# Kernel tuning notes

Measured on AMD Instinct MI355X. Metric: run time of the kernel, lower is better.

## Reference

```python
import jax, jax.numpy as jnp
import numpy as np

D = 768
H = 16
DK = D // H
DFF = 3072
POOL = 100
NCLS = 7
EPS = 1e-6


def layer_norm(x, a, b):
    # torch: (x - mean) / (std + eps), std unbiased (ddof=1)
    mean = jnp.mean(x, axis=-1, keepdims=True)
    var = jnp.sum((x - mean) ** 2, axis=-1, keepdims=True) / (x.shape[-1] - 1)
    return a * (x - mean) / (jnp.sqrt(var) + EPS) + b


def mha(x, Wq, bq, Wk, bk, Wv, bv, Wo, bo):
    B, S, _ = x.shape
    def split(h):
        return h.reshape(B, S, H, DK).transpose(0, 2, 1, 3)  # [B,H,S,DK]
    q = split(x @ Wq + bq)
    k = split(x @ Wk + bk)
    v = split(x @ Wv + bv)
    scores = jnp.einsum('bhqd,bhkd->bhqk', q, k) / jnp.sqrt(jnp.float32(DK))
    p = jax.nn.softmax(scores, axis=-1)
    o = jnp.einsum('bhqk,bhkd->bhqd', p, v)
    o = o.transpose(0, 2, 1, 3).reshape(B, S, D)
    return o @ Wo + bo


def setup_inputs() -> dict:
    key = jax.random.key(0)
    ks = jax.random.split(key, 24)
    B, S = 8, 1023
    s = 0.02
    inp = {
        'text_features': jax.random.normal(ks[0], (B, S, D), jnp.float32),
        'prompt_pool': jax.random.normal(ks[1], (POOL, D), jnp.float32),
        'cls_token': jax.random.normal(ks[2], (1, 1, D), jnp.float32),
        'Wq': jax.random.normal(ks[3], (D, D), jnp.float32) * s,
        'bq': jnp.zeros((D,), jnp.float32),
        'Wk': jax.random.normal(ks[4], (D, D), jnp.float32) * s,
        'bk': jnp.zeros((D,), jnp.float32),
        'Wv': jax.random.normal(ks[5], (D, D), jnp.float32) * s,
        'bv': jnp.zeros((D,), jnp.float32),
        'Wo': jax.random.normal(ks[6], (D, D), jnp.float32) * s,
        'bo': jnp.zeros((D,), jnp.float32),
        'ln1_a': jnp.ones((D,), jnp.float32),
        'ln1_b': jnp.zeros((D,), jnp.float32),
        'ln2_a': jnp.ones((D,), jnp.float32),
        'ln2_b': jnp.zeros((D,), jnp.float32),
        'W1': jax.random.normal(ks[7], (D, DFF), jnp.float32) * s,
        'b1': jnp.zeros((DFF,), jnp.float32),
        'W2': jax.random.normal(ks[8], (DFF, D), jnp.float32) * s,
        'b2': jnp.zeros((D,), jnp.float32),
        'lnf_a': jnp.ones((D,), jnp.float32),
        'lnf_b': jnp.zeros((D,), jnp.float32),
        'Wpool': jax.random.normal(ks[9], (D, POOL), jnp.float32) * s,
        'bpool': jnp.zeros((POOL,), jnp.float32),
        'Wcls': jax.random.normal(ks[10], (D, NCLS), jnp.float32) * s,
        'bcls': jnp.zeros((NCLS,), jnp.float32),
    }
    return inp


def reference(text_features, prompt_pool, cls_token, Wq, bq, Wk, bk, Wv, bv, Wo, bo,
              ln1_a, ln1_b, ln2_a, ln2_b, W1, b1, W2, b2, lnf_a, lnf_b,
              Wpool, bpool, Wcls, bcls):
    B = text_features.shape[0]
    x = jnp.concatenate([jnp.broadcast_to(cls_token, (B, 1, D)), text_features], axis=1)
    # EncoderLayer (N=1), dropout in eval mode (identity)
    x = x + mha(layer_norm(x, ln1_a, ln1_b), Wq, bq, Wk, bk, Wv, bv, Wo, bo)
    h = layer_norm(x, ln2_a, ln2_b)
    x = x + (jax.nn.relu(h @ W1 + b1) @ W2 + b2)
    x = layer_norm(x, lnf_a, lnf_b)
    cls = x[:, 0, :]  # [B, D]
    probabilities = jax.nn.softmax(cls @ Wpool + bpool, axis=1)  # [B, POOL]
    class_logits = cls @ Wcls + bcls  # [B, NCLS]
    class_probs = jax.nn.softmax(class_logits, axis=1)
    entropy = -jnp.sum(class_probs * jnp.log(class_probs + 1e-9), axis=1)
    max_entropy = jnp.log(jnp.float32(7.0))
    norm_ent = entropy / max_entropy
    adjusted_k = jnp.clip(jnp.floor(1.0 + norm_ent * (POOL - 1)).astype(jnp.int32), 1, POOL)  # [B]
    # full descending top-k (jit-friendly: pad to POOL instead of data-dependent max_k)
    _, top_idx = jax.lax.top_k(probabilities, POOL)  # [B, POOL]
    gathered = prompt_pool[top_idx]  # [B, POOL, D]
    keep = (jnp.arange(POOL)[None, :] < adjusted_k[:, None]).astype(prompt_pool.dtype)
    selected_prompts = gathered * keep[:, :, None]
    return (selected_prompts, class_logits)
```

## Files before the change

### kernel.cpp

```cpp
#include <hip/hip_runtime.h>


#define OUT_CLS_OFF 614400

__device__ __forceinline__ float bsum256(float v, float* red) {
    int lane = threadIdx.x & 63, w = threadIdx.x >> 6;
#pragma unroll
    for (int off = 1; off < 64; off <<= 1) v += __shfl_xor(v, off);
    __syncthreads();
    if (lane == 0) red[w] = v;
    __syncthreads();
    return red[0] + red[1] + red[2] + red[3];
}

__global__ __launch_bounds__(256) void prep_a(
    const float* __restrict__ clsT, const float* __restrict__ ga,
    const float* __restrict__ gb, const float* __restrict__ Wq,
    const float* __restrict__ bq, const float* __restrict__ Wk,
    float* __restrict__ q0, float* __restrict__ colw, int* __restrict__ cnts)
{
    __shared__ float ys[768];
    __shared__ float red[4];
    __shared__ float4 partA[16][17];
    __shared__ float4 partB[16][17];
    int t = threadIdx.x;
    if (blockIdx.x == 0 && t < 16) cnts[t] = 0;
    if (blockIdx.x < 12) {
        float a0 = clsT[t], a1 = clsT[t + 256], a2 = clsT[t + 512];
        float mean = bsum256(a0 + a1 + a2, red) * (1.0f / 768.0f);
        float d0 = a0 - mean, d1 = a1 - mean, d2 = a2 - mean;
        float var = bsum256(d0 * d0 + d1 * d1 + d2 * d2, red) * (1.0f / 767.0f);
        float den = sqrtf(var) + 1e-6f;
        ys[t]       = (ga[t] * d0) / den + gb[t];
        ys[t + 256] = (ga[t + 256] * d1) / den + gb[t + 256];
        ys[t + 512] = (ga[t + 512] * d2) / den + gb[t + 512];
        __syncthreads();
        int c = blockIdx.x * 64 + (t & 15) * 4;
        int kq = t >> 4;
        float4 acc = {0.f, 0.f, 0.f, 0.f};
#pragma unroll 8
        for (int i = 0; i < 48; ++i) {
            int k = kq * 48 + i;
            float4 w = *(const float4*)&Wq[(size_t)k * 768 + c];
            float y = ys[k];
            acc.x = fmaf(y, w.x, acc.x); acc.y = fmaf(y, w.y, acc.y);
            acc.z = fmaf(y, w.z, acc.z); acc.w = fmaf(y, w.w, acc.w);
        }
        partA[kq][t & 15] = acc;
        __syncthreads();
        if (t < 16) {
            float4 s = {0.f, 0.f, 0.f, 0.f};
#pragma unroll
            for (int i = 0; i < 16; ++i) {
                float4 v = partA[i][t];
                s.x += v.x; s.y += v.y; s.z += v.z; s.w += v.w;
            }
            int cc = blockIdx.x * 64 + t * 4;
            float4 b4 = *(const float4*)&bq[cc];
            q0[cc] = s.x + b4.x; q0[cc + 1] = s.y + b4.y;
            q0[cc + 2] = s.z + b4.z; q0[cc + 3] = s.w + b4.w;
        }
    } else {
        int c = (blockIdx.x - 12) * 64 + (t & 15) * 4;
        int kq = t >> 4;
        float4 aa = {0.f, 0.f, 0.f, 0.f}, ab = {0.f, 0.f, 0.f, 0.f};
#pragma unroll 8
        for (int i = 0; i < 48; ++i) {
            int k = kq * 48 + i;
            float4 w = *(const float4*)&Wk[(size_t)k * 768 + c];
            float g = ga[k], h = gb[k];
            aa.x = fmaf(g, w.x, aa.x); aa.y = fmaf(g, w.y, aa.y);
            aa.z = fmaf(g, w.z, aa.z); aa.w = fmaf(g, w.w, aa.w);
            ab.x = fmaf(h, w.x, ab.x); ab.y = fmaf(h, w.y, ab.y);
            ab.z = fmaf(h, w.z, ab.z); ab.w = fmaf(h, w.w, ab.w);
        }
        partA[kq][t & 15] = aa;
        partB[kq][t & 15] = ab;
        __syncthreads();
        if (t < 16) {
            float4 sa = {0.f, 0.f, 0.f, 0.f}, sb = {0.f, 0.f, 0.f, 0.f};
#pragma unroll
            for (int i = 0; i < 16; ++i) {
                float4 va = partA[i][t], vb = partB[i][t];
                sa.x += va.x; sa.y += va.y; sa.z += va.z; sa.w += va.w;
                sb.x += vb.x; sb.y += vb.y; sb.z += vb.z; sb.w += vb.w;
            }
            int cc = (blockIdx.x - 12) * 64 + t * 4;
            *(float4*)&colw[cc] = sa;
            *(float4*)&colw[768 + cc] = sb;
        }
    }
}

__global__ __launch_bounds__(256) void prep_b(
    const float* __restrict__ Wk, const float* __restrict__ bk,
    const float* __restrict__ q0, const float* __restrict__ colw,
    float* __restrict__ wkqc)
{
    __shared__ float qs[768];
    int t = threadIdx.x;
    qs[t] = q0[t]; qs[t + 256] = q0[t + 256]; qs[t + 512] = q0[t + 512];
    __syncthreads();
    const float invs = 0.14433756729740643f;
    int kl = t >> 4, h = t & 15;
    int k = blockIdx.x * 16 + kl;
    const float* wr = Wk + (size_t)k * 768 + h * 48;
    const float* qh = qs + h * 48;
    float a = 0.f;
#pragma unroll
    for (int d = 0; d < 48; d += 4) {
        float4 w = *(const float4*)&wr[d];
        a += w.x * qh[d] + w.y * qh[d + 1] + w.z * qh[d + 2] + w.w * qh[d + 3];
    }
    wkqc[k * 16 + h] = a * invs;
    if (blockIdx.x == 0 && t < 16) {
        float cd = 0.f, sa = 0.f, sb = 0.f;
        for (int d = 0; d < 48; ++d) {
            int dd = t * 48 + d;
            cd = fmaf(bk[dd], qs[dd], cd);
            sa = fmaf(colw[dd], qs[dd], sa);
            sb = fmaf(colw[768 + dd], qs[dd], sb);
        }
        wkqc[12304 + t] = sa * invs;
        wkqc[12320 + t] = sb * invs + cd * invs;
    }
}

__global__ __launch_bounds__(256) void score_upart(
    const float* __restrict__ tf, const float* __restrict__ clsT,
    const float* __restrict__ ga, const float* __restrict__ wkqc,
    float* __restrict__ up, float* __restrict__ upz, float* __restrict__ upc1)
{
    __shared__ float tr[256][17];
    __shared__ float partw[4][16];
    __shared__ float red[2][4][2];
    __shared__ float wrow[16];
    int t = threadIdx.x;
    int l = t & 63, w = t >> 6;

    float wk0[16], wk1[16], wk2[16];
    {
        const float4* p0 = (const float4*)(wkqc + t * 16);
        const float4* p1 = (const float4*)(wkqc + (t + 256) * 16);
        const float4* p2 = (const float4*)(wkqc + (t + 512) * 16);
#pragma unroll
        for (int q = 0; q < 4; ++q) {
            float4 v0 = p0[q], v1 = p1[q], v2 = p2[q];
            wk0[q * 4] = v0.x; wk0[q * 4 + 1] = v0.y; wk0[q * 4 + 2] = v0.z; wk0[q * 4 + 3] = v0.w;
            wk1[q * 4] = v1.x; wk1[q * 4 + 1] = v1.y; wk1[q * 4 + 2] = v1.z; wk1[q * 4 + 3] = v1.w;
            wk2[q * 4] = v2.x; wk2[q * 4 + 1] = v2.y; wk2[q * 4 + 2] = v2.z; wk2[q * 4 + 3] = v2.w;
        }
    }
    float ga0 = ga[t], ga1 = ga[t + 256], ga2 = ga[t + 512];
    float Sg = wkqc[12304 + (t & 15)];
    float Cg = wkqc[12320 + (t & 15)];

    float acc0[16], acc1[16], acc2[16];
#pragma unroll
    for (int h = 0; h < 16; ++h) { acc0[h] = 0.f; acc1[h] = 0.f; acc2[h] = 0.f; }
    float zacc = 0.f, c1acc = 0.f;

    int b = blockIdx.x & 7, jc = blockIdx.x >> 3;
    int j0 = jc * 32;
    const float* src0 = j0 ? (tf + ((size_t)b * 1023 + (j0 - 1)) * 768) : clsT;
    float x0 = src0[t], x1 = src0[t + 256], x2 = src0[t + 512];

    for (int r = 0; r < 32; ++r) {
        int j = j0 + r;
        float cx0 = x0, cx1 = x1, cx2 = x2;
        if (r < 31) {
            const float* sp = tf + ((size_t)b * 1023 + j) * 768;
            x0 = sp[t]; x1 = sp[t + 256]; x2 = sp[t + 512];
        }
        float s1 = cx0 + cx1 + cx2;
        float s2 = fmaf(cx0, cx0, fmaf(cx1, cx1, cx2 * cx2));
        float g0 = ga0 * cx0, g1 = ga1 * cx1, g2 = ga2 * cx2;
        {
            float dt[16];
#pragma unroll
            for (int h = 0; h < 16; ++h)
                dt[h] = fmaf(g0, wk0[h], fmaf(g1, wk1[h], g2 * wk2[h]));
#pragma unroll
            for (int off = 1; off < 64; off <<= 1) {
                s1 += __shfl_xor(s1, off);
                s2 += __shfl_xor(s2, off);
            }
            if (l == 0) { red[r & 1][w][0] = s1; red[r & 1][w][1] = s2; }
#pragma unroll
            for (int h = 0; h < 16; ++h) tr[t][h] = dt[h];
        }
        __syncthreads();
        {
            int hh = t & 15, ch = t >> 4;
            float v = 0.f;
#pragma unroll
            for (int i = 0; i < 16; ++i) v += tr[ch * 16 + i][hh];
            v += __shfl_xor(v, 16);
            v += __shfl_xor(v, 32);
            if (l < 16) partw[w][l] = v;
        }
        __syncthreads();
        if (t < 16) {
            float dtot = partw[0][t] + partw[1][t] + partw[2][t] + partw[3][t];
            float s1t = red[r & 1][0][0] + red[r & 1][1][0] + red[r & 1][2][0] + red[r & 1][3][0];
            float s2t = red[r & 1][0][1] + red[r & 1][1][1] + red[r & 1][2][1] + red[r & 1][3][1];
            float mean = s1t * (1.0f / 768.0f);
            float var = (s2t - mean * s1t) * (1.0f / 767.0f);
            float rden = 1.0f / (sqrtf(var) + 1e-6f);
            float sv = rden * (dtot - mean * Sg) + Cg;
            float e = expf(sv);
            float wv = e * rden;
            wrow[t] = wv;
            zacc += e;
            c1acc = fmaf(wv, mean, c1acc);
        }
        __syncthreads();
#pragma unroll
        for (int h = 0; h < 16; ++h) {
            float wh = wrow[h];
            acc0[h] = fmaf(wh, cx0, acc0[h]);
            acc1[h] = fmaf(wh, cx1, acc1[h]);
            acc2[h] = fmaf(wh, cx2, acc2[h]);
        }
    }

    float* o = up + (((size_t)b * 32 + jc) * 16) * 768;
#pragma unroll
    for (int h = 0; h < 16; ++h) {
        o[h * 768 + t] = acc0[h];
        o[h * 768 + t + 256] = acc1[h];
        o[h * 768 + t + 512] = acc2[h];
    }
    if (t < 16) {
        upz[((size_t)b * 32 + jc) * 16 + t] = zacc;
        upc1[((size_t)b * 32 + jc) * 16 + t] = c1acc;
    }
}

__global__ __launch_bounds__(256) void o0_k(
    const float* __restrict__ up, const float* __restrict__ upz,
    const float* __restrict__ upc1, const float* __restrict__ ga,
    const float* __restrict__ gb, const float* __restrict__ Wv,
    const float* __restrict__ bv, float* __restrict__ o0)
{
    __shared__ float us[768];
    __shared__ float part[4][64];
    int h = blockIdx.x, b = blockIdx.y, t = threadIdx.x;
    float s0 = 0.f, s1 = 0.f, s2 = 0.f;
#pragma unroll 8
    for (int jc = 0; jc < 32; ++jc) {
        const float* q = up + (((size_t)b * 32 + jc) * 16 + h) * 768;
        s0 += q[t]; s1 += q[t + 256]; s2 += q[t + 512];
    }
    float Z = 0.f, c1r = 0.f;
#pragma unroll 8
    for (int jc = 0; jc < 32; ++jc) {
        Z   += upz[((size_t)b * 32 + jc) * 16 + h];
        c1r += upc1[((size_t)b * 32 + jc) * 16 + h];
    }
    float rz = 1.0f / Z;
    us[t]       = ga[t] * ((s0 - c1r) * rz) + gb[t];
    us[t + 256] = ga[t + 256] * ((s1 - c1r) * rz) + gb[t + 256];
    us[t + 512] = ga[t + 512] * ((s2 - c1r) * rz) + gb[t + 512];
    __syncthreads();
    int dd = t & 63, kg = t >> 6;
    float a = 0.f;
    if (dd < 48) {
#pragma unroll 8
        for (int i = 0; i < 192; ++i) {
            int k = kg * 192 + i;
            a = fmaf(us[k], Wv[(size_t)k * 768 + h * 48 + dd], a);
        }
    }
    part[kg][dd] = a;
    __syncthreads();
    if (t < 48)
        o0[(size_t)b * 768 + h * 48 + t] =
            part[0][t] + part[1][t] + part[2][t] + part[3][t] + bv[h * 48 + t];
}

__global__ __launch_bounds__(256) void x2_k(
    const float* __restrict__ o0, const float* __restrict__ Wo,
    const float* __restrict__ bo, const float* __restrict__ clsT,
    float* __restrict__ x2w)
{
    __shared__ float ys[768];
    __shared__ float4 part[16][17];
    int b = blockIdx.y, t = threadIdx.x;
    const float* xr = o0 + (size_t)b * 768;
    ys[t] = xr[t]; ys[t + 256] = xr[t + 256]; ys[t + 512] = xr[t + 512];
    __syncthreads();
    int c = blockIdx.x * 64 + (t & 15) * 4;
    int kq = t >> 4;
    float4 acc = {0.f, 0.f, 0.f, 0.f};
#pragma unroll 8
    for (int i = 0; i < 48; ++i) {
        int k = kq * 48 + i;
        float4 w = *(const float4*)&Wo[(size_t)k * 768 + c];
        float y = ys[k];
        acc.x = fmaf(y, w.x, acc.x); acc.y = fmaf(y, w.y, acc.y);
        acc.z = fmaf(y, w.z, acc.z); acc.w = fmaf(y, w.w, acc.w);
    }
    part[kq][t & 15] = acc;
    __syncthreads();
    if (t < 16) {
        float4 s = {0.f, 0.f, 0.f, 0.f};
#pragma unroll
        for (int i = 0; i < 16; ++i) {
            float4 v = part[i][t];
            s.x += v.x; s.y += v.y; s.z += v.z; s.w += v.w;
        }
        int cc = blockIdx.x * 64 + t * 4;
        float4 b4 = *(const float4*)&bo[cc];
        float4 r4 = *(const float4*)&clsT[cc];
        float* o = x2w + (size_t)b * 768 + cc;
        o[0] = s.x + b4.x + r4.x; o[1] = s.y + b4.y + r4.y;
        o[2] = s.z + b4.z + r4.z; o[3] = s.w + b4.w + r4.w;
    }
}

__global__ __launch_bounds__(256) void f1_k(
    const float* __restrict__ x2w, const float* __restrict__ ga,
    const float* __restrict__ gb, const float* __restrict__ W1,
    const float* __restrict__ b1, float* __restrict__ f1w)
{
    __shared__ float ys[768];
    __shared__ float red[4];
    __shared__ float4 part[8][33];
    int b = blockIdx.y, t = threadIdx.x;
    const float* xr = x2w + (size_t)b * 768;
    float a0 = xr[t], a1 = xr[t + 256], a2 = xr[t + 512];
    float mean = bsum256(a0 + a1 + a2, red) * (1.0f / 768.0f);
    float d0 = a0 - mean, d1 = a1 - mean, d2 = a2 - mean;
    float var = bsum256(d0 * d0 + d1 * d1 + d2 * d2, red) * (1.0f / 767.0f);
    float den = sqrtf(var) + 1e-6f;
    ys[t]       = (ga[t] * d0) / den + gb[t];
    ys[t + 256] = (ga[t + 256] * d1) / den + gb[t + 256];
    ys[t + 512] = (ga[t + 512] * d2) / den + gb[t + 512];
    __syncthreads();
    int c = blockIdx.x * 128 + (t & 31) * 4;
    int kq = t >> 5;
    float4 acc = {0.f, 0.f, 0.f, 0.f};
#pragma unroll 8
    for (int i = 0; i < 96; ++i) {
        int k = kq * 96 + i;
        float4 w = *(const float4*)&W1[(size_t)k * 3072 + c];
        float y = ys[k];
        acc.x = fmaf(y, w.x, acc.x); acc.y = fmaf(y, w.y, acc.y);
        acc.z = fmaf(y, w.z, acc.z); acc.w = fmaf(y, w.w, acc.w);
    }
    part[kq][t & 31] = acc;
    __syncthreads();
    if (t < 32) {
        float4 s = {0.f, 0.f, 0.f, 0.f};
#pragma unroll
        for (int i = 0; i < 8; ++i) {
            float4 v = part[i][t];
            s.x += v.x; s.y += v.y; s.z += v.z; s.w += v.w;
        }
        int cc = blockIdx.x * 128 + t * 4;
        float4 b4 = *(const float4*)&b1[cc];
        float* o = f1w + (size_t)b * 3072 + cc;
        o[0] = fmaxf(s.x + b4.x, 0.f); o[1] = fmaxf(s.y + b4.y, 0.f);
        o[2] = fmaxf(s.z + b4.z, 0.f); o[3] = fmaxf(s.w + b4.w, 0.f);
    }
}

__global__ __launch_bounds__(256) void x3_k(
    const float* __restrict__ f1w, const float* __restrict__ W2,
    const float* __restrict__ b2, const float* __restrict__ x2w,
    float* __restrict__ x3w)
{
    __shared__ float ys[3072];
    __shared__ float4 part[16][17];
    int b = blockIdx.y, t = threadIdx.x;
    const float* xr = f1w + (size_t)b * 3072;
    for (int i = t; i < 3072; i += 256) ys[i] = xr[i];
    __syncthreads();
    int c = blockIdx.x * 64 + (t & 15) * 4;
    int kq = t >> 4;
    float4 acc = {0.f, 0.f, 0.f, 0.f};
#pragma unroll 8
    for (int i = 0; i < 192; ++i) {
        int k = kq * 192 + i;
        float4 w = *(const float4*)&W2[(size_t)k * 768 + c];
        float y = ys[k];
        acc.x = fmaf(y, w.x, acc.x); acc.y = fmaf(y, w.y, acc.y);
        acc.z = fmaf(y, w.z, acc.z); acc.w = fmaf(y, w.w, acc.w);
    }
    part[kq][t & 15] = acc;
    __syncthreads();
    if (t < 16) {
        float4 s = {0.f, 0.f, 0.f, 0.f};
#pragma unroll
        for (int i = 0; i < 16; ++i) {
            float4 v = part[i][t];
            s.x += v.x; s.y += v.y; s.z += v.z; s.w += v.w;
        }
        int cc = blockIdx.x * 64 + t * 4;
        float4 b4 = *(const float4*)&b2[cc];
        const float* x2r = x2w + (size_t)b * 768 + cc;
        float* o = x3w + (size_t)b * 768 + cc;
        o[0] = x2r[0] + s.x + b4.x; o[1] = x2r[1] + s.y + b4.y;
        o[2] = x2r[2] + s.z + b4.z; o[3] = x2r[3] + s.w + b4.w;
    }
}

__global__ __launch_bounds__(256) void logits_part(
    const float* __restrict__ x3w, const float* __restrict__ ga,
    const float* __restrict__ gb, const float* __restrict__ Wpool,
    const float* __restrict__ Wcls, double* __restrict__ lp,
    const float* __restrict__ bpool, const float* __restrict__ bcls,
    float* __restrict__ out, int* __restrict__ topw, int* __restrict__ kkw,
    int* __restrict__ cnts)
{
    __shared__ float ys[768];
    __shared__ float red[4];
    __shared__ double sPd[100];
    __shared__ double sC7d[7];
    __shared__ int sOld;
    int kg = blockIdx.x, b = blockIdx.y, t = threadIdx.x;
    const float* xr = x3w + (size_t)b * 768;
    float a0 = xr[t], a1 = xr[t + 256], a2 = xr[t + 512];
    float mean = bsum256(a0 + a1 + a2, red) * (1.0f / 768.0f);
    float d0 = a0 - mean, d1 = a1 - mean, d2 = a2 - mean;
    float var = bsum256(d0 * d0 + d1 * d1 + d2 * d2, red) * (1.0f / 767.0f);
    float den = sqrtf(var) + 1e-6f;
    ys[t]       = (ga[t] * d0) / den + gb[t];
    ys[t + 256] = (ga[t + 256] * d1) / den + gb[t + 256];
    ys[t + 512] = (ga[t + 512] * d2) / den + gb[t + 512];
    __syncthreads();
    int kbase = kg * 96;
    if (t < 100) {
        double a = 0.0;
#pragma unroll 8
        for (int i = 0; i < 96; ++i) {
            int k = kbase + i;
            a = fma((double)ys[k], (double)Wpool[k * 100 + t], a);
        }
        lp[((size_t)b * 8 + kg) * 112 + t] = a;
    } else if (t < 107) {
        int c = t - 100;
        double a = 0.0;
#pragma unroll 8
        for (int i = 0; i < 96; ++i) {
            int k = kbase + i;
            a = fma((double)ys[k], (double)Wcls[k * 7 + c], a);
        }
        lp[((size_t)b * 8 + kg) * 112 + t] = a;
    }

    __syncthreads();
    __threadfence();
    if (t == 0)
        sOld = __hip_atomic_fetch_add(&cnts[b], 1, __ATOMIC_ACQ_REL,
                                      __HIP_MEMORY_SCOPE_AGENT);
    __syncthreads();
    if (sOld != 7) return;

    if (t < 107) {
        double a = (t < 100) ? (double)bpool[t] : (double)bcls[t - 100];
#pragma unroll
        for (int g = 0; g < 8; ++g) a += lp[((size_t)b * 8 + g) * 112 + t];
        if (t < 100) sPd[t] = a;
        else {
            sC7d[t - 100] = a;
            out[OUT_CLS_OFF + b * 7 + (t - 100)] = (float)a;
        }
    }
    __syncthreads();
    if (t == 0) {
        double m7 = sC7d[0];
        for (int j = 1; j < 7; ++j) m7 = fmax(m7, sC7d[j]);
        double es[7]; double z = 0.0;
        for (int j = 0; j < 7; ++j) { es[j] = exp(sC7d[j] - m7); z += es[j]; }
        double ent = 0.0;
        for (int j = 0; j < 7; ++j) { double pr = es[j] / z; ent -= pr * log(pr + 1e-9); }
        double ne = ent / log(7.0);
        int kk = (int)floor(1.0 + ne * 99.0);
        kkw[b] = kk < 1 ? 1 : (kk > 100 ? 100 : kk);
    }
    if (t < 100) {
        double pi = sPd[t];
        int r = 0;
#pragma unroll 4
        for (int j = 0; j < 100; ++j) {
            double pj = sPd[j];
            r += (pj > pi) || (pj == pi && j < t);
        }
        topw[b * 100 + r] = t;
    }
}

__global__ __launch_bounds__(192) void gather_k(
    const float* __restrict__ pool, const int* __restrict__ topw,
    const int* __restrict__ kkw, float* __restrict__ out)
{
    int r = blockIdx.x, b = blockIdx.y, t = threadIdx.x;
    int idx = topw[b * 100 + r];
    bool keep = r < kkw[b];
    const float4* src = (const float4*)(pool + (size_t)idx * 768);
    float4* dst = (float4*)(out + (size_t)b * 76800 + (size_t)r * 768);
    float4 z = {0.f, 0.f, 0.f, 0.f};
    dst[t] = keep ? src[t] : z;
}

extern "C" void kernel_launch(void* const* d_in, const int* in_sizes, int n_in,
                              void* d_out, int out_size, void* d_ws, size_t ws_size,
                              hipStream_t stream) {
    (void)in_sizes; (void)n_in; (void)out_size; (void)ws_size;
    const float* tf    = (const float*)d_in[0];
    const float* pool  = (const float*)d_in[1];
    const float* clsT  = (const float*)d_in[2];
    const float* Wq    = (const float*)d_in[3];
    const float* bq    = (const float*)d_in[4];
    const float* Wk    = (const float*)d_in[5];
    const float* bk    = (const float*)d_in[6];
    const float* Wv    = (const float*)d_in[7];
    const float* bv    = (const float*)d_in[8];
    const float* Wo    = (const float*)d_in[9];
    const float* bo    = (const float*)d_in[10];
    const float* ln1a  = (const float*)d_in[11];
    const float* ln1b  = (const float*)d_in[12];
    const float* ln2a  = (const float*)d_in[13];
    const float* ln2b  = (const float*)d_in[14];
    const float* W1    = (const float*)d_in[15];
    const float* b1    = (const float*)d_in[16];
    const float* W2    = (const float*)d_in[17];
    const float* b2    = (const float*)d_in[18];
    const float* lnfa  = (const float*)d_in[19];
    const float* lnfb  = (const float*)d_in[20];
    const float* Wpool = (const float*)d_in[21];
    const float* bpool = (const float*)d_in[22];
    const float* Wcls  = (const float*)d_in[23];
    const float* bcls  = (const float*)d_in[24];
    float* out = (float*)d_out;
    char* ws = (char*)d_ws;

    float*  wkqc  = (float*)(ws + 0);
    float*  q0    = (float*)(ws + 49408);
    float*  colw  = (float*)(ws + 52480);
    float*  up    = (float*)(ws + 58624);
    float*  upz   = (float*)(ws + 12641536);
    float*  upc1  = (float*)(ws + 12657920);
    float*  o0    = (float*)(ws + 12674304);
    float*  x2w   = (float*)(ws + 12698880);
    float*  f1w   = (float*)(ws + 12723456);
    float*  x3w   = (float*)(ws + 12821760);
    int*    topw  = (int*)(ws + 12846336);
    int*    kkw   = (int*)(ws + 12849536);
    double* lp    = (double*)(ws + 12849568);
    int*    cnts  = (int*)(ws + 12906912);

    prep_a<<<24, 256, 0, stream>>>(clsT, ln1a, ln1b, Wq, bq, Wk, q0, colw, cnts);
    prep_b<<<48, 256, 0, stream>>>(Wk, bk, q0, colw, wkqc);
    score_upart<<<256, 256, 0, stream>>>(tf, clsT, ln1a, wkqc, up, upz, upc1);
    o0_k<<<dim3(16, 8), 256, 0, stream>>>(up, upz, upc1, ln1a, ln1b, Wv, bv, o0);
    x2_k<<<dim3(12, 8), 256, 0, stream>>>(o0, Wo, bo, clsT, x2w);
    f1_k<<<dim3(24, 8), 256, 0, stream>>>(x2w, ln2a, ln2b, W1, b1, f1w);
    x3_k<<<dim3(12, 8), 256, 0, stream>>>(f1w, W2, b2, x2w, x3w);
    logits_part<<<dim3(8, 8), 256, 0, stream>>>(x3w, lnfa, lnfb, Wpool, Wcls,
                                                lp, bpool, bcls, out, topw,
                                                kkw, cnts);
    gather_k<<<dim3(100, 8), 192, 0, stream>>>(pool, topw, kkw, out);
}
```

Before: 115.6 us.

## Halve score_upart chunk size, double grid, and defer accumulation to drop a barrier

Splits the 1024-row sequence into 64 chunks of 16 rows per batch, so score_upart launches 512 blocks instead of 256 and more of the GPU's compute units have work. The weighted-accumulate step for each row moves to the next iteration using a double-buffered wrow, which removes one __syncthreads per row. It also adds a launch-bounds occupancy hint. The cost is twice as many partial buffers (workspace offsets shift) and a 64-way reduction in o0_k instead of 32-way.

```diff
diff --git a/kernel.cpp b/kernel.cpp
--- a/kernel.cpp
+++ b/kernel.cpp
@@ -126,7 +126,7 @@
     }
 }
 
-__global__ __launch_bounds__(256) void score_upart(
+__global__ __launch_bounds__(256, 2) void score_upart(
     const float* __restrict__ tf, const float* __restrict__ clsT,
     const float* __restrict__ ga, const float* __restrict__ wkqc,
     float* __restrict__ up, float* __restrict__ upz, float* __restrict__ upc1)
@@ -134,7 +134,7 @@
     __shared__ float tr[256][17];
     __shared__ float partw[4][16];
     __shared__ float red[2][4][2];
-    __shared__ float wrow[16];
+    __shared__ float wrow[2][16];
     int t = threadIdx.x;
     int l = t & 63, w = t >> 6;
 
@@ -161,20 +161,21 @@
     float zacc = 0.f, c1acc = 0.f;
 
     int b = blockIdx.x & 7, jc = blockIdx.x >> 3;
-    int j0 = jc * 32;
+    int j0 = jc * 16;
     const float* src0 = j0 ? (tf + ((size_t)b * 1023 + (j0 - 1)) * 768) : clsT;
-    float x0 = src0[t], x1 = src0[t + 256], x2 = src0[t + 512];
-
-    for (int r = 0; r < 32; ++r) {
+    float xc0 = src0[t], xc1 = src0[t + 256], xc2 = src0[t + 512];
+    float xp0 = 0.f, xp1 = 0.f, xp2 = 0.f;
+
+    for (int r = 0; r < 16; ++r) {
         int j = j0 + r;
-        float cx0 = x0, cx1 = x1, cx2 = x2;
-        if (r < 31) {
+        float s1 = xc0 + xc1 + xc2;
+        float s2 = fmaf(xc0, xc0, fmaf(xc1, xc1, xc2 * xc2));
+        float g0 = ga0 * xc0, g1 = ga1 * xc1, g2 = ga2 * xc2;
+        float xn0 = 0.f, xn1 = 0.f, xn2 = 0.f;
+        if (r < 15) {
             const float* sp = tf + ((size_t)b * 1023 + j) * 768;
-            x0 = sp[t]; x1 = sp[t + 256]; x2 = sp[t + 512];
-        }
-        float s1 = cx0 + cx1 + cx2;
-        float s2 = fmaf(cx0, cx0, fmaf(cx1, cx1, cx2 * cx2));
-        float g0 = ga0 * cx0, g1 = ga1 * cx1, g2 = ga2 * cx2;
+            xn0 = sp[t]; xn1 = sp[t + 256]; xn2 = sp[t + 512];
+        }
         {
             float dt[16];
 #pragma unroll
@@ -190,6 +191,15 @@
             for (int h = 0; h < 16; ++h) tr[t][h] = dt[h];
         }
         __syncthreads();
+        if (r > 0) {
+#pragma unroll
+            for (int h = 0; h < 16; ++h) {
+                float wh = wrow[(r - 1) & 1][h];
+                acc0[h] = fmaf(wh, xp0, acc0[h]);
+                acc1[h] = fmaf(wh, xp1, acc1[h]);
+                acc2[h] = fmaf(wh, xp2, acc2[h]);
+            }
+        }
         {
             int hh = t & 15, ch = t >> 4;
             float v = 0.f;
@@ -210,21 +220,23 @@
             float sv = rden * (dtot - mean * Sg) + Cg;
             float e = expf(sv);
             float wv = e * rden;
-            wrow[t] = wv;
+            wrow[r & 1][t] = wv;
             zacc += e;
             c1acc = fmaf(wv, mean, c1acc);
         }
-        __syncthreads();
-#pragma unroll
-        for (int h = 0; h < 16; ++h) {
-            float wh = wrow[h];
-            acc0[h] = fmaf(wh, cx0, acc0[h]);
-            acc1[h] = fmaf(wh, cx1, acc1[h]);
-            acc2[h] = fmaf(wh, cx2, acc2[h]);
-        }
-    }
-
-    float* o = up + (((size_t)b * 32 + jc) * 16) * 768;
+        xp0 = xc0; xp1 = xc1; xp2 = xc2;
+        xc0 = xn0; xc1 = xn1; xc2 = xn2;
+    }
+    __syncthreads();
+#pragma unroll
+    for (int h = 0; h < 16; ++h) {
+        float wh = wrow[15 & 1][h];
+        acc0[h] = fmaf(wh, xp0, acc0[h]);
+        acc1[h] = fmaf(wh, xp1, acc1[h]);
+        acc2[h] = fmaf(wh, xp2, acc2[h]);
+    }
+
+    float* o = up + (((size_t)b * 64 + jc) * 16) * 768;
 #pragma unroll
     for (int h = 0; h < 16; ++h) {
         o[h * 768 + t] = acc0[h];
@@ -232,8 +244,8 @@
         o[h * 768 + t + 512] = acc2[h];
     }
     if (t < 16) {
-        upz[((size_t)b * 32 + jc) * 16 + t] = zacc;
-        upc1[((size_t)b * 32 + jc) * 16 + t] = c1acc;
+        upz[((size_t)b * 64 + jc) * 16 + t] = zacc;
+        upc1[((size_t)b * 64 + jc) * 16 + t] = c1acc;
     }
 }
 
@@ -248,15 +260,15 @@
     int h = blockIdx.x, b = blockIdx.y, t = threadIdx.x;
     float s0 = 0.f, s1 = 0.f, s2 = 0.f;
 #pragma unroll 8
-    for (int jc = 0; jc < 32; ++jc) {
-        const float* q = up + (((size_t)b * 32 + jc) * 16 + h) * 768;
+    for (int jc = 0; jc < 64; ++jc) {
+        const float* q = up + (((size_t)b * 64 + jc) * 16 + h) * 768;
         s0 += q[t]; s1 += q[t + 256]; s2 += q[t + 512];
     }
     float Z = 0.f, c1r = 0.f;
 #pragma unroll 8
-    for (int jc = 0; jc < 32; ++jc) {
-        Z   += upz[((size_t)b * 32 + jc) * 16 + h];
-        c1r += upc1[((size_t)b * 32 + jc) * 16 + h];
+    for (int jc = 0; jc < 64; ++jc) {
+        Z   += upz[((size_t)b * 64 + jc) * 16 + h];
+        c1r += upc1[((size_t)b * 64 + jc) * 16 + h];
     }
     float rz = 1.0f / Z;
     us[t]       = ga[t] * ((s0 - c1r) * rz) + gb[t];
@@ -541,20 +553,20 @@
     float*  q0    = (float*)(ws + 49408);
     float*  colw  = (float*)(ws + 52480);
     float*  up    = (float*)(ws + 58624);
-    float*  upz   = (float*)(ws + 12641536);
-    float*  upc1  = (float*)(ws + 12657920);
-    float*  o0    = (float*)(ws + 12674304);
-    float*  x2w   = (float*)(ws + 12698880);
-    float*  f1w   = (float*)(ws + 12723456);
-    float*  x3w   = (float*)(ws + 12821760);
-    int*    topw  = (int*)(ws + 12846336);
-    int*    kkw   = (int*)(ws + 12849536);
-    double* lp    = (double*)(ws + 12849568);
-    int*    cnts  = (int*)(ws + 12906912);
+    float*  upz   = (float*)(ws + 25224448);
+    float*  upc1  = (float*)(ws + 25257216);
+    float*  o0    = (float*)(ws + 25289984);
+    float*  x2w   = (float*)(ws + 25314560);
+    float*  f1w   = (float*)(ws + 25339136);
+    float*  x3w   = (float*)(ws + 25437440);
+    int*    topw  = (int*)(ws + 25462016);
+    int*    kkw   = (int*)(ws + 25465216);
+    double* lp    = (double*)(ws + 25465248);
+    int*    cnts  = (int*)(ws + 25522592);
 
     prep_a<<<24, 256, 0, stream>>>(clsT, ln1a, ln1b, Wq, bq, Wk, q0, colw, cnts);
     prep_b<<<48, 256, 0, stream>>>(Wk, bk, q0, colw, wkqc);
-    score_upart<<<256, 256, 0, stream>>>(tf, clsT, ln1a, wkqc, up, upz, upc1);
+    score_upart<<<512, 256, 0, stream>>>(tf, clsT, ln1a, wkqc, up, upz, upc1);
     o0_k<<<dim3(16, 8), 256, 0, stream>>>(up, upz, upc1, ln1a, ln1b, Wv, bv, o0);
     x2_k<<<dim3(12, 8), 256, 0, stream>>>(o0, Wo, bo, clsT, x2w);
     f1_k<<<dim3(24, 8), 256, 0, stream>>>(x2w, ln2a, ln2b, W1, b1, f1w);
```

Result: faster. 107.7 us (-6.8%).
